# Kernel tuning notes

Hardware: AMD Instinct MI355X
Metric: run time of the kernel (lower is better)

Reference implementation:

```python
import jax, jax.numpy as jnp
import numpy as np

EMB_DIM = 1024
NUM_HEADS = 16
HEAD_DIM = EMB_DIM // NUM_HEADS


def _theta_vector(head_dim):
    # theta_i = 10000^(-2i/head_dim), i = 0..head_dim/2-1 (standard RoPE)
    i = jnp.arange(head_dim // 2, dtype=jnp.float32)
    return jnp.power(10000.0, -2.0 * i / head_dim)


def _apply_rope(x, cos, sin):
    # x: [B,S,H,D]; cos,sin: [B,S,1,D/2]. Pairwise 2x2 rotation per dim-pair.
    B, S, H, D = x.shape
    xp = x.reshape(B, S, H, D // 2, 2)
    x0, x1 = xp[..., 0], xp[..., 1]
    r0 = x0 * cos - x1 * sin
    r1 = x0 * sin + x1 * cos
    return jnp.stack([r0, r1], axis=-1).reshape(B, S, H, D)


def setup_inputs() -> dict:
    key = jax.random.key(0)
    ks = jax.random.split(key, 11)
    B, S = 2, 2048
    sc = 1.0 / np.sqrt(EMB_DIM)
    x = jax.random.normal(ks[0], (B, S, EMB_DIM), dtype=jnp.float32)
    positions = jnp.sort(jax.random.randint(ks[1], (B, S), 0, 8192), axis=-1)
    Wq = jax.random.normal(ks[2], (EMB_DIM, EMB_DIM), dtype=jnp.float32) * sc
    bq = jax.random.normal(ks[3], (EMB_DIM,), dtype=jnp.float32) * 0.01
    Wk = jax.random.normal(ks[4], (EMB_DIM, EMB_DIM), dtype=jnp.float32) * sc
    bk = jax.random.normal(ks[5], (EMB_DIM,), dtype=jnp.float32) * 0.01
    Wv = jax.random.normal(ks[6], (EMB_DIM, EMB_DIM), dtype=jnp.float32) * sc
    bv = jax.random.normal(ks[7], (EMB_DIM,), dtype=jnp.float32) * 0.01
    Wo = jax.random.normal(ks[8], (EMB_DIM, EMB_DIM), dtype=jnp.float32) * sc
    bo = jax.random.normal(ks[9], (EMB_DIM,), dtype=jnp.float32) * 0.01
    return {"x": x, "positions": positions, "Wq": Wq, "bq": bq, "Wk": Wk,
            "bk": bk, "Wv": Wv, "bv": bv, "Wo": Wo, "bo": bo}


def reference(x, positions, Wq, bq, Wk, bk, Wv, bv, Wo, bo):
    B, S, E = x.shape
    H, D = NUM_HEADS, HEAD_DIM
    Q = (x @ Wq + bq).reshape(B, S, H, D)
    K = (x @ Wk + bk).reshape(B, S, H, D)
    V = (x @ Wv + bv).reshape(B, S, H, D)
    theta = _theta_vector(D)                       # [D/2]
    ang = positions.astype(jnp.float32)[..., None] * theta  # [B,S,D/2]
    cos = jnp.cos(ang)[:, :, None, :]              # [B,S,1,D/2]
    sin = jnp.sin(ang)[:, :, None, :]
    Qr = _apply_rope(Q, cos, sin).transpose(0, 2, 1, 3)   # [B,H,S,D]
    Kr = _apply_rope(K, cos, sin).transpose(0, 2, 1, 3)
    Vh = V.transpose(0, 2, 1, 3)
    scores = jnp.einsum('bhqd,bhkd->bhqk', Qr, Kr) / jnp.sqrt(jnp.float32(D))
    probs = jax.nn.softmax(scores, axis=-1)
    ctx = jnp.einsum('bhqk,bhkd->bhqd', probs, Vh)
    ctx = ctx.transpose(0, 2, 1, 3).reshape(B, S, E)
    return ctx @ Wo + bo
```

## Files before the change

kernel.cpp:

```cpp
#include <hip/hip_runtime.h>
#include <hip/hip_bf16.h>
#include <math.h>

#define B_ 2
#define S_ 2048
#define E_ 1024
#define H_ 16
#define D_ 64
#define M_ 4096
#define NT2 32
#define KVB 64

typedef __bf16 bf16;
typedef __bf16 bf16x4 __attribute__((ext_vector_type(4)));
typedef __bf16 bf16x8 __attribute__((ext_vector_type(8)));
typedef float f32x4 __attribute__((ext_vector_type(4)));
typedef float f32x16 __attribute__((ext_vector_type(16)));

__device__ __forceinline__ void gload_lds16(const void* g, void* lds) {
  __builtin_amdgcn_global_load_lds(
      (const __attribute__((address_space(1))) unsigned int*)g,
      (__attribute__((address_space(3))) unsigned int*)lds, 16, 0, 0);
}

#define MFMA16(a, b, c) __builtin_amdgcn_mfma_f32_16x16x32_bf16(a, b, c, 0, 0, 0)
#define MFMA32(a, b, c) __builtin_amdgcn_mfma_f32_32x32x16_bf16(a, b, c, 0, 0, 0)

__global__ __launch_bounds__(256)
void split_f32_kernel(const float* __restrict__ in, bf16* __restrict__ hi,
                      bf16* __restrict__ lo, int n4) {
  int i = blockIdx.x * 256 + threadIdx.x;
  if (i >= n4) return;
  float4 v = ((const float4*)in)[i];
  bf16 h0 = (bf16)v.x, h1 = (bf16)v.y, h2 = (bf16)v.z, h3 = (bf16)v.w;
  bf16x4 hv = {h0, h1, h2, h3};
  bf16x4 lv = {(bf16)(v.x - (float)h0), (bf16)(v.y - (float)h1),
               (bf16)(v.z - (float)h2), (bf16)(v.w - (float)h3)};
  *(bf16x4*)(hi + 4 * (size_t)i) = hv;
  *(bf16x4*)(lo + 4 * (size_t)i) = lv;
}

__global__ __launch_bounds__(256)
void transpose_split_kernel(const float* __restrict__ W, bf16* __restrict__ Th,
                            bf16* __restrict__ Tl) {
  __shared__ float tile[32][33];
  const int tx = threadIdx.x & 31, ty = threadIdx.x >> 5;
  const int c0 = blockIdx.x * 32, r0 = blockIdx.y * 32;
#pragma unroll
  for (int i = 0; i < 4; ++i)
    tile[ty + 8 * i][tx] = W[(size_t)(r0 + ty + 8 * i) * E_ + c0 + tx];
  __syncthreads();
#pragma unroll
  for (int i = 0; i < 4; ++i) {
    int rr = ty + 8 * i;
    float v = tile[tx][rr];
    bf16 hv = (bf16)v;
    size_t oidx = (size_t)(c0 + rr) * E_ + r0 + tx;
    Th[oidx] = hv;
    Tl[oidx] = (bf16)(v - (float)hv);
  }
}

__global__ __launch_bounds__(256)
void rope_tab_kernel(const int* __restrict__ pos, float* __restrict__ cosT,
                     float* __restrict__ sinT) {
  int idx = blockIdx.x * 256 + threadIdx.x;
  int t = idx & 31, bs = idx >> 5;
  double th = pow(10000.0, -(double)(2 * t) / 64.0);
  float ang = (float)pos[bs] * (float)th;
  double a = (double)ang;
  cosT[idx] = (float)cos(a);
  sinT[idx] = (float)sin(a);
}

#define BMq 256
#define BNq 256
#define BKq 32

__global__ __launch_bounds__(512, 2)
void gemm_qkv_kernel(const bf16* __restrict__ Ah_g, const bf16* __restrict__ Al_g,
                     const bf16* __restrict__ BhQ, const bf16* __restrict__ BlQ,
                     const bf16* __restrict__ BhK, const bf16* __restrict__ BlK,
                     const bf16* __restrict__ BhV, const bf16* __restrict__ BlV,
                     const float* __restrict__ bqp, const float* __restrict__ bkp,
                     const float* __restrict__ bvp,
                     const float* __restrict__ cosT, const float* __restrict__ sinT,
                     bf16* __restrict__ Qh, bf16* __restrict__ Qlo,
                     bf16* __restrict__ Kh, bf16* __restrict__ Klo,
                     bf16* __restrict__ VTb) {
  __shared__ bf16 lA_h[2][BMq * BKq], lA_l[2][BMq * BKq];
  __shared__ bf16 lB_h[2][BNq * BKq], lB_l[2][BNq * BKq];
  const int tid = threadIdx.x;
  const int lin = blockIdx.x;
  const int cc = (lin & 7) * 24 + (lin >> 3);
  const int third = cc >> 6;
  const int rem = cc & 63;
  const int n0 = (rem >> 4) * BNq;
  const int m0 = (rem & 15) * BMq;
  const bf16* Bh_g = third == 0 ? BhQ : third == 1 ? BhK : BhV;
  const bf16* Bl_g = third == 0 ? BlQ : third == 1 ? BlK : BlV;
  const float* bias = third == 0 ? bqp : third == 1 ? bkp : bvp;
  const int wave = tid >> 6, lane = tid & 63;
  const int wr = wave >> 2, wc = wave & 3;
  const int r = lane & 31, half = lane >> 5;
  const int KD = 1024;
  const int NK = KD / BKq;

  f32x16 acc[4][2] = {};

  auto stage_pair = [&](int kt, int buf, int mm) {
    const int k0 = kt * BKq;
    const bf16* gs = mm == 0 ? Ah_g : mm == 1 ? Al_g : mm == 2 ? Bh_g : Bl_g;
    bf16* ld = mm == 0 ? &lA_h[buf][0] : mm == 1 ? &lA_l[buf][0]
             : mm == 2 ? &lB_h[buf][0] : &lB_l[buf][0];
    const int rbase = mm < 2 ? m0 : n0;
#pragma unroll
    for (int i = 0; i < 2; ++i) {
      int c = i * 512 + tid;
      int row = c >> 2, u = c & 3;
      int us = u ^ ((row >> 1) & 3);
      const char* gp =
          (const char*)(gs + (size_t)(rbase + row) * KD + k0) + us * 16;
      char* lp = (char*)ld + (size_t)(i * 512 + wave * 64) * 16;
      gload_lds16(gp, lp);
    }
  };

#pragma unroll
  for (int mm = 0; mm < 4; ++mm) stage_pair(0, 0, mm);
  asm volatile("s_waitcnt vmcnt(0)" ::: "memory");
  __builtin_amdgcn_s_barrier();

  int cur = 0;
  for (int kt = 0; kt < NK; ++kt) {
    const bool pf = (kt + 1 < NK);
    bf16x8 b_h[2][2], b_l[2][2];
#pragma unroll
    for (int p = 0; p < 4; ++p) {
      if (pf) stage_pair(kt + 1, cur ^ 1, p);
      if (p == 0) {
#pragma unroll
        for (int ni = 0; ni < 2; ++ni)
#pragma unroll
          for (int ks = 0; ks < 2; ++ks) {
            int brow = wc * 64 + ni * 32 + r;
            int boff =
                brow * 64 + ((ks * 32 + half * 16) ^ (((brow >> 1) & 3) << 4));
            b_h[ni][ks] = *(const bf16x8*)((const char*)&lB_h[cur][0] + boff);
            b_l[ni][ks] = *(const bf16x8*)((const char*)&lB_l[cur][0] + boff);
          }
      }
      bf16x8 a_h2[2], a_l2[2];
      const int arow = wr * 128 + p * 32 + r;
#pragma unroll
      for (int ks = 0; ks < 2; ++ks) {
        int aoff =
            arow * 64 + ((ks * 32 + half * 16) ^ (((arow >> 1) & 3) << 4));
        a_h2[ks] = *(const bf16x8*)((const char*)&lA_h[cur][0] + aoff);
        a_l2[ks] = *(const bf16x8*)((const char*)&lA_l[cur][0] + aoff);
      }
      __builtin_amdgcn_s_setprio(1);
#pragma unroll
      for (int ks = 0; ks < 2; ++ks)
#pragma unroll
        for (int ni = 0; ni < 2; ++ni) {
          acc[p][ni] = MFMA32(a_h2[ks], b_h[ni][ks], acc[p][ni]);
          acc[p][ni] = MFMA32(a_h2[ks], b_l[ni][ks], acc[p][ni]);
          acc[p][ni] = MFMA32(a_l2[ks], b_h[ni][ks], acc[p][ni]);
        }
      __builtin_amdgcn_s_setprio(0);
    }
    if (pf) asm volatile("s_waitcnt vmcnt(0)" ::: "memory");
    __builtin_amdgcn_s_barrier();
    cur ^= 1;
  }

#pragma unroll
  for (int mi = 0; mi < 4; ++mi)
#pragma unroll
    for (int ni = 0; ni < 2; ++ni) {
      const int gcol = n0 + wc * 64 + ni * 32 + r;
      const float bv = bias[gcol];
      if (third < 2) {
        bf16* outH = third == 0 ? Qh : Kh;
        bf16* outL = third == 0 ? Qlo : Klo;
        const int h = gcol >> 6, d = gcol & 63, tt = d >> 1;
#pragma unroll
        for (int tq = 0; tq < 4; ++tq) {
#pragma unroll
          for (int u = 0; u < 4; ++u) {
            int reg = tq * 4 + u;
            int grow = m0 + wr * 128 + mi * 32 + (u + 8 * tq + 4 * half);
            int s = grow & (S_ - 1), b = grow >> 11;
            float v = acc[mi][ni][reg] + bv;
            float other = __shfl_xor(v, 1);
            float cs = cosT[(size_t)(b * S_ + s) * NT2 + tt];
            float sn = sinT[(size_t)(b * S_ + s) * NT2 + tt];
            float vr = (d & 1) ? (other * sn + v * cs) : (v * cs - other * sn);
            if (third == 0) vr *= 0.125f;
            bf16 hv = (bf16)vr;
            bf16 lv = (bf16)(vr - (float)hv);
            size_t idx = (((size_t)(b * H_ + h)) * S_ + s) * D_ + d;
            outH[idx] = hv;
            outL[idx] = lv;
          }
        }
      } else {
        const int h = gcol >> 6, d = gcol & 63;
#pragma unroll
        for (int tq = 0; tq < 4; ++tq) {
          int grow = m0 + wr * 128 + mi * 32 + (8 * tq + 4 * half);
          int s = grow & (S_ - 1), b = grow >> 11;
          ushort4 pk;
          unsigned short* pp = (unsigned short*)&pk;
#pragma unroll
          for (int u = 0; u < 4; ++u) {
            float v = acc[mi][ni][tq * 4 + u] + bv;
            bf16 hv = (bf16)v;
            pp[u] = __builtin_bit_cast(unsigned short, hv);
          }
          *(ushort4*)((unsigned short*)VTb +
                      (((size_t)(b * H_ + h)) * D_ + d) * S_ + s) = pk;
        }
      }
    }
}

#define BMg 128
#define BNg 128
#define BKg 32

__global__ __launch_bounds__(256)
void gemm_o_kernel(const bf16* __restrict__ Ah_g, const bf16* __restrict__ Al_g,
                   const bf16* __restrict__ Bh_g, const bf16* __restrict__ Bl_g,
                   const float* __restrict__ bias, float* __restrict__ outF) {
  __shared__ bf16 lA_h[2][BMg * BKg], lA_l[2][BMg * BKg];
  __shared__ bf16 lB_h[2][BNg * BKg], lB_l[2][BNg * BKg];
  const int tid = threadIdx.x;
  const int lin = blockIdx.x;
  const int cc = (lin & 7) * 32 + (lin >> 3);
  const int nb = cc >> 5;
  const int mb = cc & 31;
  const int m0 = mb * BMg, n0 = nb * BNg;
  const int wave = tid >> 6, lane = tid & 63;
  const int wr = wave >> 1, wc = wave & 1;
  const int r = lane & 31, half = lane >> 5;
  const int KD = 1024;
  const int NK = KD / BKg;

  f32x16 acc[2][2] = {};

  auto stage_pair = [&](int kt, int buf, int p) {
    const int k0 = kt * BKg;
#pragma unroll
    for (int j = 0; j < 2; ++j) {
      int mm = p * 2 + j;
      const bf16* gs = mm == 0 ? Ah_g : mm == 1 ? Al_g : mm == 2 ? Bh_g : Bl_g;
      bf16* ld = mm == 0 ? &lA_h[buf][0] : mm == 1 ? &lA_l[buf][0]
               : mm == 2 ? &lB_h[buf][0] : &lB_l[buf][0];
      const int rbase = mm < 2 ? m0 : n0;
#pragma unroll
      for (int i = 0; i < 2; ++i) {
        int c = i * 256 + tid;
        int row = c >> 2, u = c & 3;
        int us = u ^ ((row >> 1) & 3);
        const char* gp =
            (const char*)(gs + (size_t)(rbase + row) * KD + k0) + us * 16;
        char* lp = (char*)ld + (size_t)(i * 256 + wave * 64) * 16;
        gload_lds16(gp, lp);
      }
    }
  };

#pragma unroll
  for (int p = 0; p < 2; ++p) stage_pair(0, 0, p);
  asm volatile("s_waitcnt vmcnt(0)" ::: "memory");
  __builtin_amdgcn_s_barrier();

  int cur = 0;
  for (int kt = 0; kt < NK; ++kt) {
    const bool pf = (kt + 1 < NK);
    bf16x8 b_h[2][2], b_l[2][2];
#pragma unroll
    for (int p = 0; p < 2; ++p) {
      if (pf) stage_pair(kt + 1, cur ^ 1, p);
      if (p == 0) {
#pragma unroll
        for (int ni = 0; ni < 2; ++ni)
#pragma unroll
          for (int ks = 0; ks < 2; ++ks) {
            int brow = wc * 64 + ni * 32 + r;
            int boff =
                brow * 64 + ((ks * 32 + half * 16) ^ (((brow >> 1) & 3) << 4));
            b_h[ni][ks] = *(const bf16x8*)((const char*)&lB_h[cur][0] + boff);
            b_l[ni][ks] = *(const bf16x8*)((const char*)&lB_l[cur][0] + boff);
          }
      }
      bf16x8 a_h2[2], a_l2[2];
      const int arow = wr * 64 + p * 32 + r;
#pragma unroll
      for (int ks = 0; ks < 2; ++ks) {
        int aoff =
            arow * 64 + ((ks * 32 + half * 16) ^ (((arow >> 1) & 3) << 4));
        a_h2[ks] = *(const bf16x8*)((const char*)&lA_h[cur][0] + aoff);
        a_l2[ks] = *(const bf16x8*)((const char*)&lA_l[cur][0] + aoff);
      }
      __builtin_amdgcn_s_setprio(1);
#pragma unroll
      for (int ks = 0; ks < 2; ++ks)
#pragma unroll
        for (int ni = 0; ni < 2; ++ni) {
          acc[p][ni] = MFMA32(a_h2[ks], b_h[ni][ks], acc[p][ni]);
          acc[p][ni] = MFMA32(a_h2[ks], b_l[ni][ks], acc[p][ni]);
          acc[p][ni] = MFMA32(a_l2[ks], b_h[ni][ks], acc[p][ni]);
        }
      __builtin_amdgcn_s_setprio(0);
    }
    if (pf) asm volatile("s_waitcnt vmcnt(0)" ::: "memory");
    __builtin_amdgcn_s_barrier();
    cur ^= 1;
  }

#pragma unroll
  for (int mi = 0; mi < 2; ++mi)
#pragma unroll
    for (int ni = 0; ni < 2; ++ni) {
      const int gcol = n0 + wc * 64 + ni * 32 + r;
      const float bv = bias[gcol];
#pragma unroll
      for (int tq = 0; tq < 4; ++tq)
#pragma unroll
        for (int u = 0; u < 4; ++u) {
          int grow = m0 + wr * 64 + mi * 32 + (u + 8 * tq + 4 * half);
          outF[(size_t)grow * E_ + gcol] = acc[mi][ni][tq * 4 + u] + bv;
        }
    }
}

__global__ __launch_bounds__(256)
void attn_kernel(const bf16* __restrict__ Qh, const bf16* __restrict__ Ql,
                 const bf16* __restrict__ Kh, const bf16* __restrict__ Kl,
                 const bf16* __restrict__ VT, bf16* __restrict__ Ch,
                 bf16* __restrict__ Cl) {
  __shared__ bf16 sKh[2][KVB * 64];
  __shared__ bf16 sKl[2][KVB * 64];
  __shared__ bf16 sV[2][KVB * 64];

  const int tid = threadIdx.x;
  const int wave = tid >> 6, lane = tid & 63;
  const int r = lane & 15, hq = lane >> 4;
  const int bid = blockIdx.x;
  const int swz = (bid & 7) * 64 + (bid >> 3);
  const int bh = swz >> 4, qblk = swz & 15;
  const int q0 = qblk * 128 + wave * 32;
  const size_t hb = (size_t)bh * (S_ * D_);
  const size_t vb = (size_t)bh * (D_ * S_);

  bf16x8 qh[2][2], ql[2][2];
#pragma unroll
  for (int mi = 0; mi < 2; ++mi)
#pragma unroll
    for (int ks = 0; ks < 2; ++ks) {
      size_t off = hb + (size_t)(q0 + mi * 16 + r) * D_ + ks * 32 + hq * 8;
      qh[mi][ks] = *(const bf16x8*)&Qh[off];
      ql[mi][ks] = *(const bf16x8*)&Ql[off];
    }

  float m_lane[2] = {-1e30f, -1e30f};
  float l_lane[2] = {0.f, 0.f};
  f32x4 o[2][4] = {};

  auto stageK = [&](int kt, int buf) {
    const bf16* kbh = Kh + hb + (size_t)kt * (KVB * D_);
    const bf16* kbl = Kl + hb + (size_t)kt * (KVB * D_);
#pragma unroll
    for (int i = 0; i < 2; ++i) {
      int c = i * 256 + tid;
      int ldo = (i * 256 + wave * 64) * 16;
      int cs = c ^ ((c >> 3) & 7);
      gload_lds16(kbh + cs * 8, (char*)&sKh[buf][0] + ldo);
      gload_lds16(kbl + cs * 8, (char*)&sKl[buf][0] + ldo);
    }
  };
  uint4 vld[2];
  auto loadV = [&](int kt) {
    const bf16* vbp = VT + vb + kt * KVB;
#pragma unroll
    for (int i = 0; i < 2; ++i) {
      int c = i * 256 + tid;
      int row = c >> 3, w = c & 7;
      vld[i] = *(const uint4*)(vbp + (size_t)row * S_ + w * 8);
    }
  };
  auto writeV = [&](int buf) {
#pragma unroll
    for (int i = 0; i < 2; ++i) {
      int c = i * 256 + tid;
      int row = c >> 3, w = c & 7;
      int pb0 = (w >> 2) * 32 + (w & 1) * 16 + ((w >> 1) & 1) * 4;
      char* base = (char*)&sV[buf][0] + row * 128;
      uint2 lo = {vld[i].x, vld[i].y};
      uint2 hi = {vld[i].z, vld[i].w};
      *(uint2*)(base + ((pb0 * 2) ^ ((row & 7) << 4))) = lo;
      *(uint2*)(base + (((pb0 + 8) * 2) ^ ((row & 7) << 4))) = hi;
    }
  };

  stageK(0, 0);
  loadV(0);
  writeV(0);
  __syncthreads();
  int cur = 0;

  for (int kt = 0; kt < S_ / KVB; ++kt) {
    if (kt + 1 < S_ / KVB) {
      stageK(kt + 1, cur ^ 1);
      loadV(kt + 1);
    }

    f32x4 sf[2][4] = {};
#pragma unroll
    for (int nf = 0; nf < 4; ++nf)
#pragma unroll
      for (int ks = 0; ks < 2; ++ks) {
        int kk = nf * 16 + r;
        int boff = (kk * 128 + ks * 64 + hq * 16) ^ ((kk & 7) << 4);
        bf16x8 kkh = *(const bf16x8*)((const char*)&sKh[cur][0] + boff);
        bf16x8 kkl = *(const bf16x8*)((const char*)&sKl[cur][0] + boff);
#pragma unroll
        for (int mi = 0; mi < 2; ++mi) {
          sf[mi][nf] = MFMA16(kkh, qh[mi][ks], sf[mi][nf]);
          sf[mi][nf] = MFMA16(kkh, ql[mi][ks], sf[mi][nf]);
          sf[mi][nf] = MFMA16(kkl, qh[mi][ks], sf[mi][nf]);
        }
      }

    float lmax[2];
#pragma unroll
    for (int mi = 0; mi < 2; ++mi) {
      f32x4 m4;
#pragma unroll
      for (int e = 0; e < 4; ++e)
        m4[e] = fmaxf(fmaxf(sf[mi][0][e], sf[mi][1][e]),
                      fmaxf(sf[mi][2][e], sf[mi][3][e]));
      lmax[mi] = fmaxf(fmaxf(m4[0], m4[1]), fmaxf(m4[2], m4[3]));
    }
    int need = (lmax[0] > m_lane[0] + 8.f) || (lmax[1] > m_lane[1] + 8.f);
    if (__any(need)) {
#pragma unroll
      for (int mi = 0; mi < 2; ++mi) {
        float mx = lmax[mi];
        mx = fmaxf(mx, __shfl_xor(mx, 16));
        mx = fmaxf(mx, __shfl_xor(mx, 32));
        float mn = fmaxf(m_lane[mi], mx);
        float al = __expf(m_lane[mi] - mn);
        l_lane[mi] *= al;
        m_lane[mi] = mn;
        int alb = __builtin_bit_cast(int, al);
#pragma unroll
        for (int j = 0; j < 4; ++j) {
          int g = __builtin_amdgcn_ds_bpermute((hq * 4 + j) * 4, alb);
          float a = __builtin_bit_cast(float, g);
#pragma unroll
          for (int nd = 0; nd < 4; ++nd) o[mi][nd][j] *= a;
        }
      }
    }
    bf16x8 pa[2][2];
#pragma unroll
    for (int mi = 0; mi < 2; ++mi) {
      f32x4 s4 = {};
#pragma unroll
      for (int nf = 0; nf < 4; ++nf)
#pragma unroll
        for (int e = 0; e < 4; ++e) {
          float pv = __expf(sf[mi][nf][e] - m_lane[mi]);
          sf[mi][nf][e] = pv;
          s4[e] += pv;
        }
      l_lane[mi] += s4[0] + s4[1] + s4[2] + s4[3];
#pragma unroll
      for (int ks = 0; ks < 2; ++ks) {
        bf16x8 t;
#pragma unroll
        for (int e = 0; e < 4; ++e) {
          t[e] = (bf16)sf[mi][2 * ks][e];
          t[4 + e] = (bf16)sf[mi][2 * ks + 1][e];
        }
        pa[mi][ks] = t;
      }
    }

#pragma unroll
    for (int nd = 0; nd < 4; ++nd)
#pragma unroll
      for (int ks = 0; ks < 2; ++ks) {
        int dd = nd * 16 + r;
        int boff = (dd * 128 + ks * 64 + hq * 16) ^ ((dd & 7) << 4);
        bf16x8 vv = *(const bf16x8*)((const char*)&sV[cur][0] + boff);
#pragma unroll
        for (int mi = 0; mi < 2; ++mi)
          o[mi][nd] = MFMA16(pa[mi][ks], vv, o[mi][nd]);
      }

    if (kt + 1 < S_ / KVB) writeV(cur ^ 1);
    __syncthreads();
    cur ^= 1;
  }

  const int b = bh >> 4, h = bh & 15;
  float lq[2][4];
#pragma unroll
  for (int mi = 0; mi < 2; ++mi) {
    float lr = l_lane[mi];
    lr += __shfl_xor(lr, 16);
    lr += __shfl_xor(lr, 32);
    int lb = __builtin_bit_cast(int, lr);
#pragma unroll
    for (int j = 0; j < 4; ++j) {
      int g = __builtin_amdgcn_ds_bpermute((hq * 4 + j) * 4, lb);
      lq[mi][j] = __builtin_bit_cast(float, g);
    }
  }
#pragma unroll
  for (int mi = 0; mi < 2; ++mi)
#pragma unroll
    for (int nd = 0; nd < 4; ++nd)
#pragma unroll
      for (int j = 0; j < 4; ++j) {
        int s = q0 + mi * 16 + hq * 4 + j;
        int d = nd * 16 + r;
        float ov = o[mi][nd][j] / lq[mi][j];
        bf16 hv = (bf16)ov;
        bf16 lv = (bf16)(ov - (float)hv);
        size_t idx = (((size_t)(b * S_ + s)) * H_ + h) * D_ + d;
        Ch[idx] = hv;
        Cl[idx] = lv;
      }
}

extern "C" void kernel_launch(void* const* d_in, const int* in_sizes, int n_in,
                              void* d_out, int out_size, void* d_ws, size_t ws_size,
                              hipStream_t stream) {
  const float* x = (const float*)d_in[0];
  const int* pos = (const int*)d_in[1];
  const float* Wq = (const float*)d_in[2];
  const float* bq = (const float*)d_in[3];
  const float* Wk = (const float*)d_in[4];
  const float* bk = (const float*)d_in[5];
  const float* Wv = (const float*)d_in[6];
  const float* bv = (const float*)d_in[7];
  const float* Wo = (const float*)d_in[8];
  const float* bo = (const float*)d_in[9];
  float* out = (float*)d_out;

  char* p = (char*)d_ws;
  auto alloc = [&](size_t bytes) {
    char* rp = p;
    p += (bytes + 255) & ~(size_t)255;
    return rp;
  };
  const size_t XB = (size_t)M_ * E_ * sizeof(bf16);
  const size_t WB = (size_t)E_ * E_ * sizeof(bf16);
  const size_t TB = (size_t)B_ * S_ * NT2 * sizeof(float);
  bf16* Xh = (bf16*)alloc(XB);
  bf16* Xl = (bf16*)alloc(XB);
  bf16* WqTh = (bf16*)alloc(WB); bf16* WqTl = (bf16*)alloc(WB);
  bf16* WkTh = (bf16*)alloc(WB); bf16* WkTl = (bf16*)alloc(WB);
  bf16* WvTh = (bf16*)alloc(WB); bf16* WvTl = (bf16*)alloc(WB);
  bf16* WoTh = (bf16*)alloc(WB); bf16* WoTl = (bf16*)alloc(WB);
  float* cosT = (float*)alloc(TB);
  float* sinT = (float*)alloc(TB);
  bf16* Qh = (bf16*)alloc(XB); bf16* Qlo = (bf16*)alloc(XB);
  bf16* Kh = (bf16*)alloc(XB); bf16* Klo = (bf16*)alloc(XB);
  bf16* VTb = (bf16*)alloc(XB);
  bf16* Ch = Xh;
  bf16* Cl = Xl;

  split_f32_kernel<<<M_ * E_ / 4 / 256, 256, 0, stream>>>(x, Xh, Xl, M_ * E_ / 4);
  dim3 tg(32, 32);
  transpose_split_kernel<<<tg, 256, 0, stream>>>(Wq, WqTh, WqTl);
  transpose_split_kernel<<<tg, 256, 0, stream>>>(Wk, WkTh, WkTl);
  transpose_split_kernel<<<tg, 256, 0, stream>>>(Wv, WvTh, WvTl);
  transpose_split_kernel<<<tg, 256, 0, stream>>>(Wo, WoTh, WoTl);
  rope_tab_kernel<<<B_ * S_ * NT2 / 256, 256, 0, stream>>>(pos, cosT, sinT);

  gemm_qkv_kernel<<<192, 512, 0, stream>>>(Xh, Xl, WqTh, WqTl, WkTh, WkTl, WvTh,
                                           WvTl, bq, bk, bv, cosT, sinT, Qh, Qlo,
                                           Kh, Klo, VTb);

  attn_kernel<<<B_ * H_ * (S_ / 128), 256, 0, stream>>>(Qh, Qlo, Kh, Klo, VTb,
                                                        Ch, Cl);

  gemm_o_kernel<<<256, 256, 0, stream>>>(Ch, Cl, WoTh, WoTl, bo, out);
}
```

Baseline: 233.9 us.

## Concatenate split-bf16 K dimension in QKV GEMM and merge weight transposes

```diff
diff --git a/kernel.cpp b/kernel.cpp
--- a/kernel.cpp
+++ b/kernel.cpp
@@ -41,8 +41,16 @@
 }
 
 __global__ __launch_bounds__(256)
-void transpose_split_kernel(const float* __restrict__ W, bf16* __restrict__ Th,
-                            bf16* __restrict__ Tl) {
+void transpose_split4_kernel(const float* __restrict__ Wq, const float* __restrict__ Wk,
+                             const float* __restrict__ Wv, const float* __restrict__ Wo,
+                             bf16* __restrict__ Tqh, bf16* __restrict__ Tql,
+                             bf16* __restrict__ Tkh, bf16* __restrict__ Tkl,
+                             bf16* __restrict__ Tvh, bf16* __restrict__ Tvl,
+                             bf16* __restrict__ Toh, bf16* __restrict__ Tol) {
+  const int z = blockIdx.z;
+  const float* W = z == 0 ? Wq : z == 1 ? Wk : z == 2 ? Wv : Wo;
+  bf16* Th = z == 0 ? Tqh : z == 1 ? Tkh : z == 2 ? Tvh : Toh;
+  bf16* Tl = z == 0 ? Tql : z == 1 ? Tkl : z == 2 ? Tvl : Tol;
   __shared__ float tile[32][33];
   const int tx = threadIdx.x & 31, ty = threadIdx.x >> 5;
   const int c0 = blockIdx.x * 32, r0 = blockIdx.y * 32;
@@ -73,11 +81,13 @@
   sinT[idx] = (float)sin(a);
 }
 
-#define BMq 256
-#define BNq 256
-#define BKq 32
-
-__global__ __launch_bounds__(512, 2)
+#define BMc 256
+#define BNc 256
+#define BKc 64
+#define KCAT 3072
+#define NKC 48
+
+__global__ __launch_bounds__(512, 1)
 void gemm_qkv_kernel(const bf16* __restrict__ Ah_g, const bf16* __restrict__ Al_g,
                      const bf16* __restrict__ BhQ, const bf16* __restrict__ BlQ,
                      const bf16* __restrict__ BhK, const bf16* __restrict__ BlK,
@@ -88,140 +98,126 @@
                      bf16* __restrict__ Qh, bf16* __restrict__ Qlo,
                      bf16* __restrict__ Kh, bf16* __restrict__ Klo,
                      bf16* __restrict__ VTb) {
-  __shared__ bf16 lA_h[2][BMq * BKq], lA_l[2][BMq * BKq];
-  __shared__ bf16 lB_h[2][BNq * BKq], lB_l[2][BNq * BKq];
+  __shared__ bf16 lA[2][BMc * BKc];
+  __shared__ bf16 lB[2][BNc * BKc];
   const int tid = threadIdx.x;
   const int lin = blockIdx.x;
   const int cc = (lin & 7) * 24 + (lin >> 3);
   const int third = cc >> 6;
   const int rem = cc & 63;
-  const int n0 = (rem >> 4) * BNq;
-  const int m0 = (rem & 15) * BMq;
-  const bf16* Bh_g = third == 0 ? BhQ : third == 1 ? BhK : BhV;
-  const bf16* Bl_g = third == 0 ? BlQ : third == 1 ? BlK : BlV;
+  const int n0 = (rem >> 4) * BNc;
+  const int m0 = (rem & 15) * BMc;
+  const bf16* BhX = third == 0 ? BhQ : third == 1 ? BhK : BhV;
+  const bf16* BlX = third == 0 ? BlQ : third == 1 ? BlK : BlV;
   const float* bias = third == 0 ? bqp : third == 1 ? bkp : bvp;
   const int wave = tid >> 6, lane = tid & 63;
   const int wr = wave >> 2, wc = wave & 3;
-  const int r = lane & 31, half = lane >> 5;
-  const int KD = 1024;
-  const int NK = KD / BKq;
-
-  f32x16 acc[4][2] = {};
-
-  auto stage_pair = [&](int kt, int buf, int mm) {
-    const int k0 = kt * BKq;
-    const bf16* gs = mm == 0 ? Ah_g : mm == 1 ? Al_g : mm == 2 ? Bh_g : Bl_g;
-    bf16* ld = mm == 0 ? &lA_h[buf][0] : mm == 1 ? &lA_l[buf][0]
-             : mm == 2 ? &lB_h[buf][0] : &lB_l[buf][0];
-    const int rbase = mm < 2 ? m0 : n0;
-#pragma unroll
-    for (int i = 0; i < 2; ++i) {
-      int c = i * 512 + tid;
-      int row = c >> 2, u = c & 3;
-      int us = u ^ ((row >> 1) & 3);
-      const char* gp =
-          (const char*)(gs + (size_t)(rbase + row) * KD + k0) + us * 16;
-      char* lp = (char*)ld + (size_t)(i * 512 + wave * 64) * 16;
-      gload_lds16(gp, lp);
-    }
+  const int c16 = lane & 15, hq = lane >> 4;
+
+  f32x4 acc[8][4] = {};
+
+  auto stage_q = [&](int kt, int buf, int i) {
+    const int seg = kt >> 4;
+    const int kk0 = (kt & 15) * BKc;
+    const bf16* sA = (seg < 2) ? Ah_g : Al_g;
+    const bf16* sB = (seg == 1) ? BlX : BhX;
+    int c = i * 512 + tid;
+    int row = c >> 3, u = c & 7;
+    int us = u ^ (row & 7);
+    char* lpA = (char*)&lA[buf][0] + (size_t)(i * 512 + wave * 64) * 16;
+    char* lpB = (char*)&lB[buf][0] + (size_t)(i * 512 + wave * 64) * 16;
+    gload_lds16(sA + (size_t)(m0 + row) * 1024 + kk0 + us * 8, lpA);
+    gload_lds16(sB + (size_t)(n0 + row) * 1024 + kk0 + us * 8, lpB);
   };
 
 #pragma unroll
-  for (int mm = 0; mm < 4; ++mm) stage_pair(0, 0, mm);
+  for (int i = 0; i < 4; ++i) stage_q(0, 0, i);
   asm volatile("s_waitcnt vmcnt(0)" ::: "memory");
   __builtin_amdgcn_s_barrier();
 
   int cur = 0;
-  for (int kt = 0; kt < NK; ++kt) {
-    const bool pf = (kt + 1 < NK);
-    bf16x8 b_h[2][2], b_l[2][2];
+  for (int kt = 0; kt < NKC; ++kt) {
+    const bool pf = (kt + 1 < NKC);
+    bf16x8 bfr[4][2];
 #pragma unroll
     for (int p = 0; p < 4; ++p) {
-      if (pf) stage_pair(kt + 1, cur ^ 1, p);
+      if (pf) stage_q(kt + 1, cur ^ 1, p);
       if (p == 0) {
 #pragma unroll
-        for (int ni = 0; ni < 2; ++ni)
+        for (int ni = 0; ni < 4; ++ni)
 #pragma unroll
           for (int ks = 0; ks < 2; ++ks) {
-            int brow = wc * 64 + ni * 32 + r;
-            int boff =
-                brow * 64 + ((ks * 32 + half * 16) ^ (((brow >> 1) & 3) << 4));
-            b_h[ni][ks] = *(const bf16x8*)((const char*)&lB_h[cur][0] + boff);
-            b_l[ni][ks] = *(const bf16x8*)((const char*)&lB_l[cur][0] + boff);
+            int brow = wc * 64 + ni * 16 + c16;
+            int boff = brow * 128 + ((ks * 64 + hq * 16) ^ ((brow & 7) << 4));
+            bfr[ni][ks] = *(const bf16x8*)((const char*)&lB[cur][0] + boff);
           }
       }
-      bf16x8 a_h2[2], a_l2[2];
-      const int arow = wr * 128 + p * 32 + r;
-#pragma unroll
-      for (int ks = 0; ks < 2; ++ks) {
-        int aoff =
-            arow * 64 + ((ks * 32 + half * 16) ^ (((arow >> 1) & 3) << 4));
-        a_h2[ks] = *(const bf16x8*)((const char*)&lA_h[cur][0] + aoff);
-        a_l2[ks] = *(const bf16x8*)((const char*)&lA_l[cur][0] + aoff);
-      }
+      bf16x8 af[2][2];
+#pragma unroll
+      for (int s = 0; s < 2; ++s)
+#pragma unroll
+        for (int ks = 0; ks < 2; ++ks) {
+          int arow = wr * 128 + (2 * p + s) * 16 + c16;
+          int aoff = arow * 128 + ((ks * 64 + hq * 16) ^ ((arow & 7) << 4));
+          af[s][ks] = *(const bf16x8*)((const char*)&lA[cur][0] + aoff);
+        }
+      __builtin_amdgcn_s_barrier();
       __builtin_amdgcn_s_setprio(1);
 #pragma unroll
-      for (int ks = 0; ks < 2; ++ks)
-#pragma unroll
-        for (int ni = 0; ni < 2; ++ni) {
-          acc[p][ni] = MFMA32(a_h2[ks], b_h[ni][ks], acc[p][ni]);
-          acc[p][ni] = MFMA32(a_h2[ks], b_l[ni][ks], acc[p][ni]);
-          acc[p][ni] = MFMA32(a_l2[ks], b_h[ni][ks], acc[p][ni]);
-        }
+      for (int s = 0; s < 2; ++s)
+#pragma unroll
+        for (int ks = 0; ks < 2; ++ks)
+#pragma unroll
+          for (int ni = 0; ni < 4; ++ni)
+            acc[2 * p + s][ni] = MFMA16(af[s][ks], bfr[ni][ks], acc[2 * p + s][ni]);
       __builtin_amdgcn_s_setprio(0);
-    }
-    if (pf) asm volatile("s_waitcnt vmcnt(0)" ::: "memory");
+      __builtin_amdgcn_s_barrier();
+    }
+    asm volatile("s_waitcnt vmcnt(0)" ::: "memory");
     __builtin_amdgcn_s_barrier();
     cur ^= 1;
   }
 
 #pragma unroll
-  for (int mi = 0; mi < 4; ++mi)
-#pragma unroll
-    for (int ni = 0; ni < 2; ++ni) {
-      const int gcol = n0 + wc * 64 + ni * 32 + r;
+  for (int mi = 0; mi < 8; ++mi)
+#pragma unroll
+    for (int ni = 0; ni < 4; ++ni) {
+      const int gcol = n0 + wc * 64 + ni * 16 + c16;
       const float bv = bias[gcol];
       if (third < 2) {
         bf16* outH = third == 0 ? Qh : Kh;
         bf16* outL = third == 0 ? Qlo : Klo;
         const int h = gcol >> 6, d = gcol & 63, tt = d >> 1;
 #pragma unroll
-        for (int tq = 0; tq < 4; ++tq) {
-#pragma unroll
-          for (int u = 0; u < 4; ++u) {
-            int reg = tq * 4 + u;
-            int grow = m0 + wr * 128 + mi * 32 + (u + 8 * tq + 4 * half);
-            int s = grow & (S_ - 1), b = grow >> 11;
-            float v = acc[mi][ni][reg] + bv;
-            float other = __shfl_xor(v, 1);
-            float cs = cosT[(size_t)(b * S_ + s) * NT2 + tt];
-            float sn = sinT[(size_t)(b * S_ + s) * NT2 + tt];
-            float vr = (d & 1) ? (other * sn + v * cs) : (v * cs - other * sn);
-            if (third == 0) vr *= 0.125f;
-            bf16 hv = (bf16)vr;
-            bf16 lv = (bf16)(vr - (float)hv);
-            size_t idx = (((size_t)(b * H_ + h)) * S_ + s) * D_ + d;
-            outH[idx] = hv;
-            outL[idx] = lv;
-          }
+        for (int reg = 0; reg < 4; ++reg) {
+          int grow = m0 + wr * 128 + mi * 16 + hq * 4 + reg;
+          int s = grow & (S_ - 1), b = grow >> 11;
+          float v = acc[mi][ni][reg] + bv;
+          float other = __shfl_xor(v, 1);
+          float cs = cosT[(size_t)(b * S_ + s) * NT2 + tt];
+          float sn = sinT[(size_t)(b * S_ + s) * NT2 + tt];
+          float vr = (d & 1) ? (other * sn + v * cs) : (v * cs - other * sn);
+          if (third == 0) vr *= 0.125f;
+          bf16 hv = (bf16)vr;
+          bf16 lv = (bf16)(vr - (float)hv);
+          size_t idx = (((size_t)(b * H_ + h)) * S_ + s) * D_ + d;
+          outH[idx] = hv;
+          outL[idx] = lv;
         }
       } else {
         const int h = gcol >> 6, d = gcol & 63;
-#pragma unroll
-        for (int tq = 0; tq < 4; ++tq) {
-          int grow = m0 + wr * 128 + mi * 32 + (8 * tq + 4 * half);
-          int s = grow & (S_ - 1), b = grow >> 11;
-          ushort4 pk;
-          unsigned short* pp = (unsigned short*)&pk;
-#pragma unroll
-          for (int u = 0; u < 4; ++u) {
-            float v = acc[mi][ni][tq * 4 + u] + bv;
-            bf16 hv = (bf16)v;
-            pp[u] = __builtin_bit_cast(unsigned short, hv);
-          }
-          *(ushort4*)((unsigned short*)VTb +
-                      (((size_t)(b * H_ + h)) * D_ + d) * S_ + s) = pk;
-        }
+        int grow = m0 + wr * 128 + mi * 16 + hq * 4;
+        int s = grow & (S_ - 1), b = grow >> 11;
+        ushort4 pk;
+        unsigned short* pp = (unsigned short*)&pk;
+#pragma unroll
+        for (int reg = 0; reg < 4; ++reg) {
+          float v = acc[mi][ni][reg] + bv;
+          bf16 hv = (bf16)v;
+          pp[reg] = __builtin_bit_cast(unsigned short, hv);
+        }
+        *(ushort4*)((unsigned short*)VTb +
+                    (((size_t)(b * H_ + h)) * D_ + d) * S_ + s) = pk;
       }
     }
 }
@@ -578,11 +574,10 @@
   bf16* Cl = Xl;
 
   split_f32_kernel<<<M_ * E_ / 4 / 256, 256, 0, stream>>>(x, Xh, Xl, M_ * E_ / 4);
-  dim3 tg(32, 32);
-  transpose_split_kernel<<<tg, 256, 0, stream>>>(Wq, WqTh, WqTl);
-  transpose_split_kernel<<<tg, 256, 0, stream>>>(Wk, WkTh, WkTl);
-  transpose_split_kernel<<<tg, 256, 0, stream>>>(Wv, WvTh, WvTl);
-  transpose_split_kernel<<<tg, 256, 0, stream>>>(Wo, WoTh, WoTl);
+  dim3 tg(32, 32, 4);
+  transpose_split4_kernel<<<tg, 256, 0, stream>>>(Wq, Wk, Wv, Wo, WqTh, WqTl,
+                                                  WkTh, WkTl, WvTh, WvTl, WoTh,
+                                                  WoTl);
   rope_tab_kernel<<<B_ * S_ * NT2 / 256, 256, 0, stream>>>(pos, cosT, sinT);
 
   gemm_qkv_kernel<<<192, 512, 0, stream>>>(Xh, Xl, WqTh, WqTl, WkTh, WkTl, WvTh,
```

New measurement: 292.8 us. 1.25x slower.
